# Performance work log

Measured on AMD Instinct MI355X. Metric: run time of the kernel, lower is better.

Reference implementation:

```python
import jax, jax.numpy as jnp
import numpy as np

N = 50000
E = 800000
IN, HID, OUT = 256, 64, 64
H1, H2 = 4, 1
SLOPE = 0.2  # DGL GATConv default negative_slope


def setup_inputs() -> dict:
    key = jax.random.key(0)
    ks = jax.random.split(key, 12)
    inp = {
        "features": jax.random.normal(ks[0], (N, IN), jnp.float32),
        "src": jax.random.randint(ks[1], (E,), 0, N),
        "dst": jax.random.randint(ks[2], (E,), 0, N),
        # layer 1 params (fc has no bias in DGL; separate bias added post-aggregation)
        "W1": jax.random.normal(ks[3], (IN, H1 * HID), jnp.float32) * (1.0 / np.sqrt(IN)),
        "al1": jax.random.normal(ks[4], (H1, HID), jnp.float32) * 0.1,
        "ar1": jax.random.normal(ks[5], (H1, HID), jnp.float32) * 0.1,
        "b1": jnp.zeros((H1 * HID,), jnp.float32),
        # layer 2 params
        "W2": jax.random.normal(ks[6], (H1 * HID, H2 * OUT), jnp.float32) * (1.0 / np.sqrt(H1 * HID)),
        "al2": jax.random.normal(ks[7], (H2, OUT), jnp.float32) * 0.1,
        "ar2": jax.random.normal(ks[8], (H2, OUT), jnp.float32) * 0.1,
        "b2": jnp.zeros((H2 * OUT,), jnp.float32),
    }
    return inp


def _gat_layer(x, src, dst, W, al, ar, b, H, D):
    # fc projection + reshape to [N, H, D]
    h = (x @ W).reshape(-1, H, D)
    el = jnp.einsum("nhd,hd->nh", h, al)  # [N,H]
    er = jnp.einsum("nhd,hd->nh", h, ar)
    e = jax.nn.leaky_relu(el[src] + er[dst], SLOPE)  # [E,H]
    # segment (per-dst-node) softmax over incoming edges
    emax = jax.ops.segment_max(e, dst, num_segments=N)
    ex = jnp.exp(e - emax[dst])
    denom = jax.ops.segment_sum(ex, dst, num_segments=N)
    a = ex / denom[dst]  # [E,H]
    # weighted gather-scatter aggregation
    out = jax.ops.segment_sum(a[:, :, None] * h[src], dst, num_segments=N)  # [N,H,D]
    return out + b.reshape(1, H, D)


def reference(features, src, dst, W1, al1, ar1, b1, W2, al2, ar2, b2):
    # layer 1: GATConv + elu activation, then flatten heads
    h = _gat_layer(features, src, dst, W1, al1, ar1, b1, H1, HID)
    h = jax.nn.elu(h).reshape(N, H1 * HID)
    # layer 2: GATConv (no activation), then mean over heads
    h = _gat_layer(h, src, dst, W2, al2, ar2, b2, H2, OUT)
    return h.mean(axis=1)  # [N, OUT]
```

## Files before the change

kernel.cpp:

```cpp
#include <hip/hip_runtime.h>
#include <hip/hip_bf16.h>
#include <hip/hip_fp16.h>
#include <math.h>

#define SLOPE 0.2f

typedef __attribute__((ext_vector_type(8))) short bf16x8;
typedef __attribute__((ext_vector_type(4))) float f32x4;

__device__ inline unsigned short f2bf(float f) {
    unsigned u = __float_as_uint(f);
    u += 0x7FFF + ((u >> 16) & 1);
    return (unsigned short)(u >> 16);
}
__device__ inline float bf2f(unsigned short s) {
    return __uint_as_float(((unsigned)s) << 16);
}
__device__ inline unsigned cvt_pk_bf16(float a, float b) {
    unsigned r;
    asm("v_cvt_pk_bf16_f32 %0, %1, %2" : "=v"(r) : "v"(a), "v"(b));
    return r;
}


__global__ void deg_cvtw_kernel(const int* __restrict__ dst, int* __restrict__ deg,
                                int* __restrict__ rank, int E,
                                const float* __restrict__ W1,
                                const float* __restrict__ W2,
                                unsigned short* __restrict__ Wt1,
                                unsigned short* __restrict__ Wt2) {
    if (blockIdx.x < 256) {
        const int k = blockIdx.x, c = threadIdx.x;
        Wt1[c * 256 + k] = f2bf(W1[k * 256 + c]);
        if (c < 64) Wt2[c * 256 + k] = f2bf(W2[k * 64 + c]);
    } else {
        const int i = (blockIdx.x - 256) * blockDim.x + threadIdx.x;
        if (i < E) rank[i] = atomicAdd(&deg[dst[i]], 1);
    }
}

__global__ __launch_bounds__(256) void psum_kernel(const int* __restrict__ deg,
                                                   int* __restrict__ bsum, int n) {
    const int t = threadIdx.x;
    const int i = blockIdx.x * 256 + t;
    int v = (i < n) ? deg[i] : 0;
#pragma unroll
    for (int o = 1; o < 64; o <<= 1) v += __shfl_xor(v, o, 64);
    __shared__ int ws[4];
    if ((t & 63) == 0) ws[t >> 6] = v;
    __syncthreads();
    if (t == 0) bsum[blockIdx.x] = ws[0] + ws[1] + ws[2] + ws[3];
}

__global__ __launch_bounds__(256) void scan2_kernel(const int* __restrict__ deg,
                                                    const int* __restrict__ bsum,
                                                    int* __restrict__ offs, int n) {
    const int b = blockIdx.x, t = threadIdx.x;
    const int lane = t & 63, w = t >> 6;

    int contrib = (t < b) ? bsum[t] : 0;
#pragma unroll
    for (int o = 1; o < 64; o <<= 1) contrib += __shfl_xor(contrib, o, 64);
    __shared__ int wsum[4];
    if (lane == 0) wsum[w] = contrib;
    __syncthreads();
    const int base = wsum[0] + wsum[1] + wsum[2] + wsum[3];

    const int i = b * 256 + t;
    const int v = (i < n) ? deg[i] : 0;
    int incl = v;
#pragma unroll
    for (int o = 1; o < 64; o <<= 1) {
        const int u = __shfl_up(incl, o, 64);
        if (lane >= o) incl += u;
    }
    __shared__ int wtot[4];
    if (lane == 63) wtot[w] = incl;
    __syncthreads();
    int wbase = 0;
#pragma unroll
    for (int k = 0; k < 4; ++k)
        if (k < w) wbase += wtot[k];

    const int excl = base + wbase + incl - v;
    if (i < n) offs[i] = excl;
    if (i == n - 1) offs[n] = excl + v;
}

__global__ __launch_bounds__(256) void gemm1_fill(const float* __restrict__ Xf,
                                                  const unsigned short* __restrict__ Wt,
                                                  const float* __restrict__ AL,
                                                  const float* __restrict__ AR,
                                                  unsigned short* __restrict__ Hout,
                                                  float* __restrict__ el,
                                                  float* __restrict__ er, int n, int GB,
                                                  const int* __restrict__ src,
                                                  const int* __restrict__ dst,
                                                  const int* __restrict__ offs,
                                                  const int* __restrict__ rank,
                                                  int* __restrict__ csr_src, int E) {
    constexpr int LDR = 72;
    __shared__ __align__(16) unsigned short Xs[128 * LDR];
    __shared__ __align__(16) unsigned short Ws[256 * LDR];

    if (blockIdx.x >= GB) {
        const int i = (blockIdx.x - GB) * blockDim.x + threadIdx.x;
        if (i < E) csr_src[offs[dst[i]] + rank[i]] = src[i];
        return;
    }

    const int tid = threadIdx.x;
    const int wave = tid >> 6, lane = tid & 63;
    const int col16 = lane & 15, quad = lane >> 4;
    const int node0 = blockIdx.x * 128;

    f32x4 acc[16][2];
#pragma unroll
    for (int ft = 0; ft < 16; ++ft)
#pragma unroll
        for (int nt = 0; nt < 2; ++nt) acc[ft][nt] = (f32x4){0.f, 0.f, 0.f, 0.f};

    const int rr = tid >> 3;
    const int cc = (tid & 7) * 8;

    for (int k0 = 0; k0 < 256; k0 += 64) {
#pragma unroll
        for (int p = 0; p < 4; ++p) {
            const int row = rr + p * 32;
            int gx = node0 + row; if (gx >= n) gx = n - 1;
            const float4* xp = (const float4*)&Xf[(long long)gx * 256 + k0 + cc];
            const float4 a = xp[0];
            const float4 b = xp[1];
            uint4 pk;
            pk.x = cvt_pk_bf16(a.x, a.y);
            pk.y = cvt_pk_bf16(a.z, a.w);
            pk.z = cvt_pk_bf16(b.x, b.y);
            pk.w = cvt_pk_bf16(b.z, b.w);
            *(uint4*)&Xs[row * LDR + cc] = pk;
        }
#pragma unroll
        for (int p = 0; p < 8; ++p) {
            const int row = rr + p * 32;
            *(bf16x8*)&Ws[row * LDR + cc] =
                *(const bf16x8*)&Wt[(long long)row * 256 + k0 + cc];
        }
        __syncthreads();
#pragma unroll
        for (int ks = 0; ks < 64; ks += 32) {
            bf16x8 bfrag[2];
#pragma unroll
            for (int nt = 0; nt < 2; ++nt)
                bfrag[nt] = *(const bf16x8*)&Xs[(wave * 32 + nt * 16 + col16) * LDR +
                                                ks + quad * 8];
#pragma unroll
            for (int ft = 0; ft < 16; ++ft) {
                const bf16x8 afrag =
                    *(const bf16x8*)&Ws[(ft * 16 + col16) * LDR + ks + quad * 8];
                acc[ft][0] = __builtin_amdgcn_mfma_f32_16x16x32_bf16(afrag, bfrag[0],
                                                                     acc[ft][0], 0, 0, 0);
                acc[ft][1] = __builtin_amdgcn_mfma_f32_16x16x32_bf16(afrag, bfrag[1],
                                                                     acc[ft][1], 0, 0, 0);
            }
        }
        __syncthreads();
    }

    float elp[2][4] = {{0.f}, {0.f}};
    float erp[2][4] = {{0.f}, {0.f}};
#pragma unroll
    for (int ft = 0; ft < 16; ++ft) {
        const int hb = ft >> 2;
        float alw[4], arw[4];
#pragma unroll
        for (int r = 0; r < 4; ++r) {
            const int d = (ft & 3) * 16 + quad * 4 + r;
            alw[r] = AL[hb * 64 + d];
            arw[r] = AR[hb * 64 + d];
        }
#pragma unroll
        for (int nt = 0; nt < 2; ++nt) {
            const int node = node0 + wave * 32 + nt * 16 + col16;
            if (node < n) {
                uint2 pk;
                pk.x = cvt_pk_bf16(acc[ft][nt][0], acc[ft][nt][1]);
                pk.y = cvt_pk_bf16(acc[ft][nt][2], acc[ft][nt][3]);
                *(uint2*)&Hout[(long long)node * 256 + ft * 16 + quad * 4] = pk;
            }
#pragma unroll
            for (int r = 0; r < 4; ++r) {
                elp[nt][hb] = fmaf(acc[ft][nt][r], alw[r], elp[nt][hb]);
                erp[nt][hb] = fmaf(acc[ft][nt][r], arw[r], erp[nt][hb]);
            }
        }
    }
#pragma unroll
    for (int nt = 0; nt < 2; ++nt)
#pragma unroll
        for (int hb = 0; hb < 4; ++hb) {
            elp[nt][hb] += __shfl_xor(elp[nt][hb], 16, 64);
            elp[nt][hb] += __shfl_xor(elp[nt][hb], 32, 64);
            erp[nt][hb] += __shfl_xor(erp[nt][hb], 16, 64);
            erp[nt][hb] += __shfl_xor(erp[nt][hb], 32, 64);
        }
    if (quad == 0) {
#pragma unroll
        for (int nt = 0; nt < 2; ++nt) {
            const int node = node0 + wave * 32 + nt * 16 + col16;
            if (node < n) {
#pragma unroll
                for (int hb = 0; hb < 4; ++hb) {
                    el[node * 4 + hb] = elp[nt][hb];
                    er[node * 4 + hb] = erp[nt][hb];
                }
            }
        }
    }
}

__global__ __launch_bounds__(256) void gemm2_mfma(const unsigned short* __restrict__ Xbf,
                                                  const unsigned short* __restrict__ Wt,
                                                  const float* __restrict__ AL,
                                                  const float* __restrict__ AR,
                                                  unsigned short* __restrict__ Hout,
                                                  float* __restrict__ el,
                                                  float* __restrict__ er, int n) {
    constexpr int LDR = 72;
    __shared__ __align__(16) unsigned short Xs[128 * LDR];
    __shared__ __align__(16) unsigned short Ws[64 * LDR];

    const int tid = threadIdx.x;
    const int wave = tid >> 6, lane = tid & 63;
    const int col16 = lane & 15, quad = lane >> 4;
    const int node0 = blockIdx.x * 128;

    f32x4 acc[4][2];
#pragma unroll
    for (int ft = 0; ft < 4; ++ft)
#pragma unroll
        for (int nt = 0; nt < 2; ++nt) acc[ft][nt] = (f32x4){0.f, 0.f, 0.f, 0.f};

    const int rr = tid >> 3;
    const int cc = (tid & 7) * 8;

    for (int k0 = 0; k0 < 256; k0 += 64) {
#pragma unroll
        for (int p = 0; p < 4; ++p) {
            const int row = rr + p * 32;
            int gx = node0 + row; if (gx >= n) gx = n - 1;
            *(bf16x8*)&Xs[row * LDR + cc] =
                *(const bf16x8*)&Xbf[(long long)gx * 256 + k0 + cc];
        }
#pragma unroll
        for (int p = 0; p < 2; ++p) {
            const int row = rr + p * 32;
            *(bf16x8*)&Ws[row * LDR + cc] =
                *(const bf16x8*)&Wt[(long long)row * 256 + k0 + cc];
        }
        __syncthreads();
#pragma unroll
        for (int ks = 0; ks < 64; ks += 32) {
            bf16x8 bfrag[2];
#pragma unroll
            for (int nt = 0; nt < 2; ++nt)
                bfrag[nt] = *(const bf16x8*)&Xs[(wave * 32 + nt * 16 + col16) * LDR +
                                                ks + quad * 8];
#pragma unroll
            for (int ft = 0; ft < 4; ++ft) {
                const bf16x8 afrag =
                    *(const bf16x8*)&Ws[(ft * 16 + col16) * LDR + ks + quad * 8];
                acc[ft][0] = __builtin_amdgcn_mfma_f32_16x16x32_bf16(afrag, bfrag[0],
                                                                     acc[ft][0], 0, 0, 0);
                acc[ft][1] = __builtin_amdgcn_mfma_f32_16x16x32_bf16(afrag, bfrag[1],
                                                                     acc[ft][1], 0, 0, 0);
            }
        }
        __syncthreads();
    }

    float elp[2] = {0.f, 0.f}, erp[2] = {0.f, 0.f};
#pragma unroll
    for (int ft = 0; ft < 4; ++ft) {
        float alw[4], arw[4];
#pragma unroll
        for (int r = 0; r < 4; ++r) {
            const int d = ft * 16 + quad * 4 + r;
            alw[r] = AL[d];
            arw[r] = AR[d];
        }
#pragma unroll
        for (int nt = 0; nt < 2; ++nt) {
            const int node = node0 + wave * 32 + nt * 16 + col16;
            if (node < n) {
                ushort4 pk;
                pk.x = __half_as_ushort(__float2half(acc[ft][nt][0]));
                pk.y = __half_as_ushort(__float2half(acc[ft][nt][1]));
                pk.z = __half_as_ushort(__float2half(acc[ft][nt][2]));
                pk.w = __half_as_ushort(__float2half(acc[ft][nt][3]));
                *(ushort4*)&Hout[(long long)node * 64 + ft * 16 + quad * 4] = pk;
            }
#pragma unroll
            for (int r = 0; r < 4; ++r) {
                elp[nt] = fmaf(acc[ft][nt][r], alw[r], elp[nt]);
                erp[nt] = fmaf(acc[ft][nt][r], arw[r], erp[nt]);
            }
        }
    }
#pragma unroll
    for (int nt = 0; nt < 2; ++nt) {
        elp[nt] += __shfl_xor(elp[nt], 16, 64);
        elp[nt] += __shfl_xor(elp[nt], 32, 64);
        erp[nt] += __shfl_xor(erp[nt], 16, 64);
        erp[nt] += __shfl_xor(erp[nt], 32, 64);
    }
    if (quad == 0) {
#pragma unroll
        for (int nt = 0; nt < 2; ++nt) {
            const int node = node0 + wave * 32 + nt * 16 + col16;
            if (node < n) {
                el[node] = elp[nt];
                er[node] = erp[nt];
            }
        }
    }
}

__global__ __launch_bounds__(256) void aggr1_kernel(const unsigned short* __restrict__ Hf,
                                                    const float* __restrict__ el,
                                                    const float* __restrict__ er,
                                                    const int* __restrict__ offs,
                                                    const int* __restrict__ csr,
                                                    const float* __restrict__ bias,
                                                    unsigned short* __restrict__ out,
                                                    int n) {
    const int node = (blockIdx.x * blockDim.x + threadIdx.x) >> 6;
    if (node >= n) return;
    const int lane = threadIdx.x & 63;
    const int g = lane >> 4;
    const int r = lane & 15;
    const int h = r >> 2;
    const int beg = offs[node], end = offs[node + 1];
    const float erv = er[node * 4 + h];

    float acc[16];
#pragma unroll
    for (int q = 0; q < 16; ++q) acc[q] = 0.f;
    float l = 0.f;

    const int nb = (end - beg + 3) >> 2;
    int ci = beg + g; if (ci >= end) ci = end - 1;
    int s = csr[ci];
#pragma unroll 2
    for (int it = 0; it < nb; ++it) {
        const int ei = beg + it * 4 + g;
        const bool ok = ei < end;
        int nci = ei + 4; if (nci >= end) nci = end - 1;
        const int sn = csr[nci];
        float e = el[s * 4 + h] + erv;
        e = (e > 0.f) ? e : SLOPE * e;
        float p = __expf(fminf(e, 80.f));
        if (!ok) p = 0.f;
        const uint4* hp = (const uint4*)(Hf + (s << 8) + (r << 4));
        const uint4 u0 = hp[0];
        const uint4 u1 = hp[1];
        l += p;
        const unsigned uu[8] = {u0.x, u0.y, u0.z, u0.w, u1.x, u1.y, u1.z, u1.w};
#pragma unroll
        for (int q = 0; q < 8; ++q) {
            const float flo = __uint_as_float(uu[q] << 16);
            const float fhi = __uint_as_float(uu[q] & 0xFFFF0000u);
            acc[2 * q]     = fmaf(p, flo, acc[2 * q]);
            acc[2 * q + 1] = fmaf(p, fhi, acc[2 * q + 1]);
        }
        s = sn;
    }

#pragma unroll
    for (int q = 0; q < 16; ++q) {
        acc[q] += __shfl_xor(acc[q], 16, 64);
        acc[q] += __shfl_xor(acc[q], 32, 64);
    }
    l += __shfl_xor(l, 16, 64);
    l += __shfl_xor(l, 32, 64);

    if (g == 0) {
        const float inv = (l > 0.f) ? 1.f / l : 0.f;
        unsigned o[8];
#pragma unroll
        for (int q = 0; q < 8; ++q) {
            float v0 = acc[2 * q]     * inv + bias[r * 16 + 2 * q];
            float v1 = acc[2 * q + 1] * inv + bias[r * 16 + 2 * q + 1];
            v0 = (v0 > 0.f) ? v0 : expm1f(v0);
            v1 = (v1 > 0.f) ? v1 : expm1f(v1);
            o[q] = cvt_pk_bf16(v0, v1);
        }
        uint4* op = (uint4*)(out + (node << 8) + (r << 4));
        op[0] = make_uint4(o[0], o[1], o[2], o[3]);
        op[1] = make_uint4(o[4], o[5], o[6], o[7]);
    }
}

__global__ __launch_bounds__(256) void aggr2_kernel(const unsigned short* __restrict__ Hf,
                                                    const float* __restrict__ el,
                                                    const float* __restrict__ er,
                                                    const int* __restrict__ offs,
                                                    const int* __restrict__ csr,
                                                    const float* __restrict__ bias,
                                                    float* __restrict__ out, int n) {
    const int node = (blockIdx.x * blockDim.x + threadIdx.x) >> 6;
    if (node >= n) return;
    const int lane = threadIdx.x & 63;
    const int g = lane >> 3;
    const int r = lane & 7;
    const int beg = offs[node], end = offs[node + 1];
    const float erv = er[node];

    float acc[8];
#pragma unroll
    for (int q = 0; q < 8; ++q) acc[q] = 0.f;
    float l = 0.f;

    const int nb = (end - beg + 7) >> 3;
    int ci = beg + g; if (ci >= end) ci = end - 1;
    int s = csr[ci];
#pragma unroll 2
    for (int it = 0; it < nb; ++it) {
        const int ei = beg + it * 8 + g;
        const bool ok = ei < end;
        int nci = ei + 8; if (nci >= end) nci = end - 1;
        const int sn = csr[nci];
        float e = el[s] + erv;
        e = (e > 0.f) ? e : SLOPE * e;
        float p = __expf(fminf(e, 80.f));
        if (!ok) p = 0.f;
        const uint4 u = *(const uint4*)(Hf + (s << 6) + (r << 3));
        l += p;
        const unsigned uu[4] = {u.x, u.y, u.z, u.w};
#pragma unroll
        for (int q = 0; q < 4; ++q) {
            const float hlo = __half2float(__ushort_as_half((unsigned short)(uu[q] & 0xFFFFu)));
            const float hhi = __half2float(__ushort_as_half((unsigned short)(uu[q] >> 16)));
            acc[2 * q]     = fmaf(p, hlo, acc[2 * q]);
            acc[2 * q + 1] = fmaf(p, hhi, acc[2 * q + 1]);
        }
        s = sn;
    }

#pragma unroll
    for (int q = 0; q < 8; ++q) {
        acc[q] += __shfl_xor(acc[q], 8, 64);
        acc[q] += __shfl_xor(acc[q], 16, 64);
        acc[q] += __shfl_xor(acc[q], 32, 64);
    }
    l += __shfl_xor(l, 8, 64);
    l += __shfl_xor(l, 16, 64);
    l += __shfl_xor(l, 32, 64);

    if (g == 0) {
        const float inv = (l > 0.f) ? 1.f / l : 0.f;
        const float4 b0 = *(const float4*)(bias + r * 8);
        const float4 b1 = *(const float4*)(bias + r * 8 + 4);
        float* op = out + (node << 6) + (r << 3);
        *(float4*)op = make_float4(fmaf(acc[0], inv, b0.x), fmaf(acc[1], inv, b0.y),
                                   fmaf(acc[2], inv, b0.z), fmaf(acc[3], inv, b0.w));
        *(float4*)(op + 4) = make_float4(fmaf(acc[4], inv, b1.x), fmaf(acc[5], inv, b1.y),
                                         fmaf(acc[6], inv, b1.z), fmaf(acc[7], inv, b1.w));
    }
}


extern "C" void kernel_launch(void* const* d_in, const int* in_sizes, int n_in,
                              void* d_out, int out_size, void* d_ws, size_t ws_size,
                              hipStream_t stream) {
    const float* feat = (const float*)d_in[0];
    const int*   src  = (const int*)d_in[1];
    const int*   dst  = (const int*)d_in[2];
    const float* W1   = (const float*)d_in[3];
    const float* al1  = (const float*)d_in[4];
    const float* ar1  = (const float*)d_in[5];
    const float* b1   = (const float*)d_in[6];
    const float* W2   = (const float*)d_in[7];
    const float* al2  = (const float*)d_in[8];
    const float* ar2  = (const float*)d_in[9];
    const float* b2   = (const float*)d_in[10];
    float* out = (float*)d_out;

    const int IN = 256, HID = 64, OUT = 64, H1 = 4, H2 = 1;
    const int N = in_sizes[0] / IN;
    const int E = in_sizes[1];

    size_t off = 0;
    auto alloc = [&](size_t bytes) {
        void* p = (char*)d_ws + off;
        off += (bytes + 255) & ~(size_t)255;
        return p;
    };
    int*   deg    = (int*)alloc((size_t)N * 4);
    int*   offs   = (int*)alloc((size_t)(N + 1) * 4);
    int*   bsum   = (int*)alloc((size_t)256 * 4);
    int*   rank   = (int*)alloc((size_t)E * 4);
    int*   csr    = (int*)alloc((size_t)E * 4);
    unsigned short* h1   = (unsigned short*)alloc((size_t)N * H1 * HID * 2);
    unsigned short* wt1  = (unsigned short*)alloc((size_t)IN * H1 * HID * 2);
    unsigned short* wt2  = (unsigned short*)alloc((size_t)H1 * HID * H2 * OUT * 2);
    unsigned short* x2bf = (unsigned short*)alloc((size_t)N * H1 * HID * 2);
    unsigned short* h2   = (unsigned short*)alloc((size_t)N * H2 * OUT * 2);
    float* el1    = (float*)alloc((size_t)N * H1 * 4);
    float* er1    = (float*)alloc((size_t)N * H1 * 4);
    float* el2    = (float*)alloc((size_t)N * H2 * 4);
    float* er2    = (float*)alloc((size_t)N * H2 * 4);
    (void)ws_size;

    hipMemsetAsync(deg, 0, (size_t)N * 4, stream);

    const int nb = (N + 255) / 256;
    const int eb = (E + 255) / 256;
    const int GB = (N + 127) / 128;

    deg_cvtw_kernel<<<256 + eb, 256, 0, stream>>>(dst, deg, rank, E, W1, W2, wt1, wt2);
    psum_kernel<<<nb, 256, 0, stream>>>(deg, bsum, N);
    scan2_kernel<<<nb, 256, 0, stream>>>(deg, bsum, offs, N);

    gemm1_fill<<<GB + eb, 256, 0, stream>>>(feat, wt1, al1, ar1, h1, el1, er1, N, GB,
                                            src, dst, offs, rank, csr, E);

    aggr1_kernel<<<(N + 3) / 4, 256, 0, stream>>>(h1, el1, er1, offs, csr, b1, x2bf, N);
    gemm2_mfma<<<(N + 127) / 128, 256, 0, stream>>>(x2bf, wt2, al2, ar2, h2, el2, er2, N);
    aggr2_kernel<<<(N + 3) / 4, 256, 0, stream>>>(h2, el2, er2, offs, csr, b2, out, N);
}
```

Measured before the change: 281.8 us.

## Fuse layer-1 aggregation with layer-2 GEMM through shared memory

Result: slower. 309.3 us (+9.8%).

```diff
diff --git a/kernel.cpp b/kernel.cpp
--- a/kernel.cpp
+++ b/kernel.cpp
@@ -217,185 +217,172 @@
     }
 }
 
-__global__ __launch_bounds__(256) void gemm2_mfma(const unsigned short* __restrict__ Xbf,
-                                                  const unsigned short* __restrict__ Wt,
-                                                  const float* __restrict__ AL,
-                                                  const float* __restrict__ AR,
-                                                  unsigned short* __restrict__ Hout,
-                                                  float* __restrict__ el,
-                                                  float* __restrict__ er, int n) {
+__global__ __launch_bounds__(512) void aggr1_gemm2(const unsigned short* __restrict__ Hf,
+                                                   const float* __restrict__ el,
+                                                   const float* __restrict__ er,
+                                                   const int* __restrict__ offs,
+                                                   const int* __restrict__ csr,
+                                                   const float* __restrict__ bias,
+                                                   const unsigned short* __restrict__ Wt2,
+                                                   const float* __restrict__ AL2,
+                                                   const float* __restrict__ AR2,
+                                                   unsigned short* __restrict__ Hout,
+                                                   float* __restrict__ el2,
+                                                   float* __restrict__ er2, int n) {
+    constexpr int LDX = 264;
     constexpr int LDR = 72;
-    __shared__ __align__(16) unsigned short Xs[128 * LDR];
+    __shared__ __align__(16) unsigned short x2s[64 * LDX];
     __shared__ __align__(16) unsigned short Ws[64 * LDR];
+    __shared__ float elq[2][64], erq[2][64];
 
     const int tid = threadIdx.x;
     const int wave = tid >> 6, lane = tid & 63;
+    const int node0 = blockIdx.x * 64;
+
+    {
+        const int g = lane >> 4;
+        const int r = lane & 15;
+        const int h = r >> 2;
+        for (int rnd = 0; rnd < 8; ++rnd) {
+            const int ln = rnd * 8 + wave;
+            const int node = node0 + ln;
+            if (node < n) {
+                const int beg = offs[node], end = offs[node + 1];
+                const float erv = er[node * 4 + h];
+                float acc[16];
+#pragma unroll
+                for (int q = 0; q < 16; ++q) acc[q] = 0.f;
+                float l = 0.f;
+                const int nb = (end - beg + 3) >> 2;
+                int ci = beg + g; if (ci >= end) ci = end - 1;
+                int s = csr[ci];
+#pragma unroll 2
+                for (int it = 0; it < nb; ++it) {
+                    const int ei = beg + it * 4 + g;
+                    const bool ok = ei < end;
+                    int nci = ei + 4; if (nci >= end) nci = end - 1;
+                    const int sn = csr[nci];
+                    float e = el[s * 4 + h] + erv;
+                    e = (e > 0.f) ? e : SLOPE * e;
+                    float p = __expf(fminf(e, 80.f));
+                    if (!ok) p = 0.f;
+                    const uint4* hp = (const uint4*)(Hf + (s << 8) + (r << 4));
+                    const uint4 u0 = hp[0];
+                    const uint4 u1 = hp[1];
+                    l += p;
+                    const unsigned uu[8] = {u0.x, u0.y, u0.z, u0.w, u1.x, u1.y, u1.z, u1.w};
+#pragma unroll
+                    for (int q = 0; q < 8; ++q) {
+                        const float flo = __uint_as_float(uu[q] << 16);
+                        const float fhi = __uint_as_float(uu[q] & 0xFFFF0000u);
+                        acc[2 * q]     = fmaf(p, flo, acc[2 * q]);
+                        acc[2 * q + 1] = fmaf(p, fhi, acc[2 * q + 1]);
+                    }
+                    s = sn;
+                }
+#pragma unroll
+                for (int q = 0; q < 16; ++q) {
+                    acc[q] += __shfl_xor(acc[q], 16, 64);
+                    acc[q] += __shfl_xor(acc[q], 32, 64);
+                }
+                l += __shfl_xor(l, 16, 64);
+                l += __shfl_xor(l, 32, 64);
+                if (g == 0) {
+                    const float inv = (l > 0.f) ? 1.f / l : 0.f;
+                    unsigned o[8];
+#pragma unroll
+                    for (int q = 0; q < 8; ++q) {
+                        float v0 = acc[2 * q]     * inv + bias[r * 16 + 2 * q];
+                        float v1 = acc[2 * q + 1] * inv + bias[r * 16 + 2 * q + 1];
+                        v0 = (v0 > 0.f) ? v0 : expm1f(v0);
+                        v1 = (v1 > 0.f) ? v1 : expm1f(v1);
+                        o[q] = cvt_pk_bf16(v0, v1);
+                    }
+                    uint4* op = (uint4*)&x2s[ln * LDX + r * 16];
+                    op[0] = make_uint4(o[0], o[1], o[2], o[3]);
+                    op[1] = make_uint4(o[4], o[5], o[6], o[7]);
+                }
+            } else if (g == 0) {
+                uint4* op = (uint4*)&x2s[ln * LDX + r * 16];
+                op[0] = make_uint4(0, 0, 0, 0);
+                op[1] = make_uint4(0, 0, 0, 0);
+            }
+        }
+    }
+    __syncthreads();
+
     const int col16 = lane & 15, quad = lane >> 4;
-    const int node0 = blockIdx.x * 128;
-
-    f32x4 acc[4][2];
-#pragma unroll
-    for (int ft = 0; ft < 4; ++ft)
-#pragma unroll
-        for (int nt = 0; nt < 2; ++nt) acc[ft][nt] = (f32x4){0.f, 0.f, 0.f, 0.f};
-
-    const int rr = tid >> 3;
-    const int cc = (tid & 7) * 8;
+    const int nt = wave & 3;
+    const int fp = wave >> 2;
+
+    f32x4 acc2[2];
+    acc2[0] = (f32x4){0.f, 0.f, 0.f, 0.f};
+    acc2[1] = (f32x4){0.f, 0.f, 0.f, 0.f};
+
+    const int wrow = tid >> 3;
+    const int wc0 = (tid & 7) * 8;
 
     for (int k0 = 0; k0 < 256; k0 += 64) {
-#pragma unroll
-        for (int p = 0; p < 4; ++p) {
-            const int row = rr + p * 32;
-            int gx = node0 + row; if (gx >= n) gx = n - 1;
-            *(bf16x8*)&Xs[row * LDR + cc] =
-                *(const bf16x8*)&Xbf[(long long)gx * 256 + k0 + cc];
-        }
-#pragma unroll
-        for (int p = 0; p < 2; ++p) {
-            const int row = rr + p * 32;
-            *(bf16x8*)&Ws[row * LDR + cc] =
-                *(const bf16x8*)&Wt[(long long)row * 256 + k0 + cc];
-        }
+        *(bf16x8*)&Ws[wrow * LDR + wc0] =
+            *(const bf16x8*)&Wt2[wrow * 256 + k0 + wc0];
         __syncthreads();
 #pragma unroll
         for (int ks = 0; ks < 64; ks += 32) {
-            bf16x8 bfrag[2];
-#pragma unroll
-            for (int nt = 0; nt < 2; ++nt)
-                bfrag[nt] = *(const bf16x8*)&Xs[(wave * 32 + nt * 16 + col16) * LDR +
-                                                ks + quad * 8];
-#pragma unroll
-            for (int ft = 0; ft < 4; ++ft) {
+            const bf16x8 bfrag =
+                *(const bf16x8*)&x2s[(nt * 16 + col16) * LDX + k0 + ks + quad * 8];
+#pragma unroll
+            for (int j = 0; j < 2; ++j) {
                 const bf16x8 afrag =
-                    *(const bf16x8*)&Ws[(ft * 16 + col16) * LDR + ks + quad * 8];
-                acc[ft][0] = __builtin_amdgcn_mfma_f32_16x16x32_bf16(afrag, bfrag[0],
-                                                                     acc[ft][0], 0, 0, 0);
-                acc[ft][1] = __builtin_amdgcn_mfma_f32_16x16x32_bf16(afrag, bfrag[1],
-                                                                     acc[ft][1], 0, 0, 0);
+                    *(const bf16x8*)&Ws[((fp * 2 + j) * 16 + col16) * LDR + ks + quad * 8];
+                acc2[j] = __builtin_amdgcn_mfma_f32_16x16x32_bf16(afrag, bfrag,
+                                                                  acc2[j], 0, 0, 0);
             }
         }
         __syncthreads();
     }
 
-    float elp[2] = {0.f, 0.f}, erp[2] = {0.f, 0.f};
-#pragma unroll
-    for (int ft = 0; ft < 4; ++ft) {
+    float elp = 0.f, erp = 0.f;
+#pragma unroll
+    for (int j = 0; j < 2; ++j) {
+        const int ft = fp * 2 + j;
         float alw[4], arw[4];
 #pragma unroll
         for (int r = 0; r < 4; ++r) {
             const int d = ft * 16 + quad * 4 + r;
-            alw[r] = AL[d];
-            arw[r] = AR[d];
-        }
-#pragma unroll
-        for (int nt = 0; nt < 2; ++nt) {
-            const int node = node0 + wave * 32 + nt * 16 + col16;
-            if (node < n) {
-                ushort4 pk;
-                pk.x = __half_as_ushort(__float2half(acc[ft][nt][0]));
-                pk.y = __half_as_ushort(__float2half(acc[ft][nt][1]));
-                pk.z = __half_as_ushort(__float2half(acc[ft][nt][2]));
-                pk.w = __half_as_ushort(__float2half(acc[ft][nt][3]));
-                *(ushort4*)&Hout[(long long)node * 64 + ft * 16 + quad * 4] = pk;
-            }
-#pragma unroll
-            for (int r = 0; r < 4; ++r) {
-                elp[nt] = fmaf(acc[ft][nt][r], alw[r], elp[nt]);
-                erp[nt] = fmaf(acc[ft][nt][r], arw[r], erp[nt]);
-            }
-        }
-    }
-#pragma unroll
-    for (int nt = 0; nt < 2; ++nt) {
-        elp[nt] += __shfl_xor(elp[nt], 16, 64);
-        elp[nt] += __shfl_xor(elp[nt], 32, 64);
-        erp[nt] += __shfl_xor(erp[nt], 16, 64);
-        erp[nt] += __shfl_xor(erp[nt], 32, 64);
-    }
+            alw[r] = AL2[d];
+            arw[r] = AR2[d];
+        }
+        const int node = node0 + nt * 16 + col16;
+        if (node < n) {
+            ushort4 pk;
+            pk.x = __half_as_ushort(__float2half(acc2[j][0]));
+            pk.y = __half_as_ushort(__float2half(acc2[j][1]));
+            pk.z = __half_as_ushort(__float2half(acc2[j][2]));
+            pk.w = __half_as_ushort(__float2half(acc2[j][3]));
+            *(ushort4*)&Hout[(long long)node * 64 + ft * 16 + quad * 4] = pk;
+        }
+#pragma unroll
+        for (int r = 0; r < 4; ++r) {
+            elp = fmaf(acc2[j][r], alw[r], elp);
+            erp = fmaf(acc2[j][r], arw[r], erp);
+        }
+    }
+    elp += __shfl_xor(elp, 16, 64);
+    elp += __shfl_xor(elp, 32, 64);
+    erp += __shfl_xor(erp, 16, 64);
+    erp += __shfl_xor(erp, 32, 64);
     if (quad == 0) {
-#pragma unroll
-        for (int nt = 0; nt < 2; ++nt) {
-            const int node = node0 + wave * 32 + nt * 16 + col16;
-            if (node < n) {
-                el[node] = elp[nt];
-                er[node] = erp[nt];
-            }
-        }
-    }
-}
-
-__global__ __launch_bounds__(256) void aggr1_kernel(const unsigned short* __restrict__ Hf,
-                                                    const float* __restrict__ el,
-                                                    const float* __restrict__ er,
-                                                    const int* __restrict__ offs,
-                                                    const int* __restrict__ csr,
-                                                    const float* __restrict__ bias,
-                                                    unsigned short* __restrict__ out,
-                                                    int n) {
-    const int node = (blockIdx.x * blockDim.x + threadIdx.x) >> 6;
-    if (node >= n) return;
-    const int lane = threadIdx.x & 63;
-    const int g = lane >> 4;
-    const int r = lane & 15;
-    const int h = r >> 2;
-    const int beg = offs[node], end = offs[node + 1];
-    const float erv = er[node * 4 + h];
-
-    float acc[16];
-#pragma unroll
-    for (int q = 0; q < 16; ++q) acc[q] = 0.f;
-    float l = 0.f;
-
-    const int nb = (end - beg + 3) >> 2;
-    int ci = beg + g; if (ci >= end) ci = end - 1;
-    int s = csr[ci];
-#pragma unroll 2
-    for (int it = 0; it < nb; ++it) {
-        const int ei = beg + it * 4 + g;
-        const bool ok = ei < end;
-        int nci = ei + 4; if (nci >= end) nci = end - 1;
-        const int sn = csr[nci];
-        float e = el[s * 4 + h] + erv;
-        e = (e > 0.f) ? e : SLOPE * e;
-        float p = __expf(fminf(e, 80.f));
-        if (!ok) p = 0.f;
-        const uint4* hp = (const uint4*)(Hf + (s << 8) + (r << 4));
-        const uint4 u0 = hp[0];
-        const uint4 u1 = hp[1];
-        l += p;
-        const unsigned uu[8] = {u0.x, u0.y, u0.z, u0.w, u1.x, u1.y, u1.z, u1.w};
-#pragma unroll
-        for (int q = 0; q < 8; ++q) {
-            const float flo = __uint_as_float(uu[q] << 16);
-            const float fhi = __uint_as_float(uu[q] & 0xFFFF0000u);
-            acc[2 * q]     = fmaf(p, flo, acc[2 * q]);
-            acc[2 * q + 1] = fmaf(p, fhi, acc[2 * q + 1]);
-        }
-        s = sn;
-    }
-
-#pragma unroll
-    for (int q = 0; q < 16; ++q) {
-        acc[q] += __shfl_xor(acc[q], 16, 64);
-        acc[q] += __shfl_xor(acc[q], 32, 64);
-    }
-    l += __shfl_xor(l, 16, 64);
-    l += __shfl_xor(l, 32, 64);
-
-    if (g == 0) {
-        const float inv = (l > 0.f) ? 1.f / l : 0.f;
-        unsigned o[8];
-#pragma unroll
-        for (int q = 0; q < 8; ++q) {
-            float v0 = acc[2 * q]     * inv + bias[r * 16 + 2 * q];
-            float v1 = acc[2 * q + 1] * inv + bias[r * 16 + 2 * q + 1];
-            v0 = (v0 > 0.f) ? v0 : expm1f(v0);
-            v1 = (v1 > 0.f) ? v1 : expm1f(v1);
-            o[q] = cvt_pk_bf16(v0, v1);
-        }
-        uint4* op = (uint4*)(out + (node << 8) + (r << 4));
-        op[0] = make_uint4(o[0], o[1], o[2], o[3]);
-        op[1] = make_uint4(o[4], o[5], o[6], o[7]);
+        elq[fp][nt * 16 + col16] = elp;
+        erq[fp][nt * 16 + col16] = erp;
+    }
+    __syncthreads();
+    if (fp == 0 && quad == 0) {
+        const int ln = nt * 16 + col16;
+        const int node = node0 + ln;
+        if (node < n) {
+            el2[node] = elq[0][ln] + elq[1][ln];
+            er2[node] = erq[0][ln] + erq[1][ln];
+        }
     }
 }
 
@@ -502,7 +489,6 @@
     unsigned short* h1   = (unsigned short*)alloc((size_t)N * H1 * HID * 2);
     unsigned short* wt1  = (unsigned short*)alloc((size_t)IN * H1 * HID * 2);
     unsigned short* wt2  = (unsigned short*)alloc((size_t)H1 * HID * H2 * OUT * 2);
-    unsigned short* x2bf = (unsigned short*)alloc((size_t)N * H1 * HID * 2);
     unsigned short* h2   = (unsigned short*)alloc((size_t)N * H2 * OUT * 2);
     float* el1    = (float*)alloc((size_t)N * H1 * 4);
     float* er1    = (float*)alloc((size_t)N * H1 * 4);
@@ -523,7 +509,8 @@
     gemm1_fill<<<GB + eb, 256, 0, stream>>>(feat, wt1, al1, ar1, h1, el1, er1, N, GB,
                                             src, dst, offs, rank, csr, E);
 
-    aggr1_kernel<<<(N + 3) / 4, 256, 0, stream>>>(h1, el1, er1, offs, csr, b1, x2bf, N);
-    gemm2_mfma<<<(N + 127) / 128, 256, 0, stream>>>(x2bf, wt2, al2, ar2, h2, el2, er2, N);
+    aggr1_gemm2<<<(N + 63) / 64, 512, 0, stream>>>(h1, el1, er1, offs, csr, b1,
+                                                   wt2, al2, ar2, h2, el2, er2, N);
+
     aggr2_kernel<<<(N + 3) / 4, 256, 0, stream>>>(h2, el2, er2, offs, csr, b2, out, N);
 }
```
